# Kernel optimization log

Hardware: AMD Instinct MI355X
Metric: run time of the kernel (lower is better)

Reference implementation:

```python
import jax, jax.numpy as jnp
import numpy as np

B, LQ, LKV, E, H, D, P = 2, 2048, 2048, 1024, 16, 64, 64
NEG = -1e10


def setup_inputs() -> dict:
    key = jax.random.key(0)
    ks = jax.random.split(key, 8)
    inputs_q = jax.random.normal(ks[0], (B, LQ, E), jnp.float32)
    inputs_kv = jax.random.normal(ks[1], (B, LKV, E), jnp.float32)
    key_prefix = jax.random.normal(ks[2], (B, P, H, D), jnp.float32)
    value_prefix = jax.random.normal(ks[3], (B, P, H, D), jnp.float32)
    # causal mask, broadcastable over heads: [B, 1, LQ, LKV]
    mask = jnp.broadcast_to(jnp.tril(jnp.ones((LQ, LKV), bool)), (B, 1, LQ, LKV))
    scale = 1.0 / np.sqrt(E)  # fan_in variance scaling
    Wq = jax.random.normal(ks[4], (E, H, D), jnp.float32) * scale
    Wk = jax.random.normal(ks[5], (E, H, D), jnp.float32) * scale
    Wv = jax.random.normal(ks[6], (E, H, D), jnp.float32) * scale
    Wo = jax.random.normal(ks[7], (H, D, E), jnp.float32) * (1.0 / np.sqrt(H * D))
    return dict(inputs_q=inputs_q, inputs_kv=inputs_kv, key_prefix=key_prefix,
                value_prefix=value_prefix, mask=mask, Wq=Wq, Wk=Wk, Wv=Wv, Wo=Wo)


def reference(inputs_q, inputs_kv, key_prefix, value_prefix, mask, Wq, Wk, Wv, Wo):
    depth_scaling = jnp.sqrt(jnp.asarray(D, inputs_q.dtype))
    # query kernel is divided by sqrt(head_dim) at init -> fold into projection
    q = jnp.einsum('bqe,ehd->bqhd', inputs_q, Wq) / depth_scaling
    k = jnp.einsum('bke,ehd->bkhd', inputs_kv, Wk)
    v = jnp.einsum('bke,ehd->bkhd', inputs_kv, Wv)
    # prefix concat on the key/value length axis
    k = jnp.concatenate([key_prefix, k], axis=1)   # [B, P+LKV, H, D]
    v = jnp.concatenate([value_prefix, v], axis=1)
    # mask -> additive bias; prefix tokens get zero bias (always attendable)
    bias = jnp.where(mask, 0.0, NEG).astype(inputs_q.dtype)      # [B,1,LQ,LKV]
    prefix_bias = jnp.zeros(bias.shape[:-1] + (P,), bias.dtype)  # [B,1,LQ,P]
    bias = jnp.concatenate([prefix_bias, bias], axis=-1)         # [B,1,LQ,P+LKV]
    scores = jnp.einsum('bqhd,bkhd->bhqk', q, k) + bias
    probs = jax.nn.softmax(scores, axis=-1)
    ctx = jnp.einsum('bhqk,bkhd->bqhd', probs, v)
    return jnp.einsum('bqhd,hde->bqe', ctx, Wo)
```

## Files before the change

kernel.cpp:

```cpp
#include <hip/hip_runtime.h>
#include <hip/hip_bf16.h>

#define B_   2
#define LQ_  2048
#define LKV_ 2048
#define E_   1024
#define H_   16
#define D_   64
#define P_   64
#define LT_  (P_ + LKV_)
#define NEG_ -1e10f
#define LOG2E_ 1.4426950408889634f

typedef unsigned short ushort_t;
typedef unsigned int   uint_t;
typedef float f32x4   __attribute__((ext_vector_type(4)));
typedef float f32x16  __attribute__((ext_vector_type(16)));
typedef short bf16x8  __attribute__((ext_vector_type(8)));
typedef uint_t u32x4  __attribute__((ext_vector_type(4)));

__device__ __forceinline__ ushort_t f2bf(float f) {
    union { float f; uint_t u; } v; v.f = f;
    return (ushort_t)((v.u + 0x7fffu + ((v.u >> 16) & 1u)) >> 16);
}

__device__ __forceinline__ uint_t cvt_pk_bf16(float lo, float hi) {
    uint_t r;
    asm("v_cvt_pk_bf16_f32 %0, %1, %2" : "=v"(r) : "v"(lo), "v"(hi));
    return r;
}

__device__ __forceinline__ float exp2x(float x) {
    float r;
    asm("v_exp_f32 %0, %1" : "=v"(r) : "v"(x));
    return r;
}

__device__ __forceinline__ float bflo(uint_t u) {
    return __builtin_bit_cast(float, u << 16);
}
__device__ __forceinline__ float bfhi(uint_t u) {
    return __builtin_bit_cast(float, u & 0xFFFF0000u);
}


#define GLOAD16(gp, lp)                                                     \
    __builtin_amdgcn_global_load_lds(                                       \
        (const __attribute__((address_space(1))) void*)(gp),                \
        (__attribute__((address_space(3))) void*)(lp), 16, 0, 0)

__global__ __launch_bounds__(256) void cast_ab(const float* __restrict__ a,
                                               const float* __restrict__ b,
                                               ushort_t* __restrict__ da,
                                               ushort_t* __restrict__ db)
{
    const int idx = blockIdx.x * 256 + threadIdx.x;
    constexpr int HALF = 4096 * 1024 / 4;
    const float4 v = (idx < HALF) ? ((const float4*)a)[idx]
                                  : ((const float4*)b)[idx - HALF];
    const uint2 p = make_uint2((uint_t)f2bf(v.x) | ((uint_t)f2bf(v.y) << 16),
                               (uint_t)f2bf(v.z) | ((uint_t)f2bf(v.w) << 16));
    if (idx < HALF) ((uint2*)da)[idx] = p;
    else            ((uint2*)db)[idx - HALF] = p;
}

__global__ __launch_bounds__(256) void transpose_cast(
    const float* __restrict__ s0, const float* __restrict__ s1,
    const float* __restrict__ s2, const float* __restrict__ s3,
    ushort_t* __restrict__ d0, ushort_t* __restrict__ d1,
    ushort_t* __restrict__ d2, ushort_t* __restrict__ d3)
{
    const float* S = (blockIdx.z == 0) ? s0 : (blockIdx.z == 1) ? s1
                     : (blockIdx.z == 2) ? s2 : s3;
    ushort_t* D = (blockIdx.z == 0) ? d0 : (blockIdx.z == 1) ? d1
                  : (blockIdx.z == 2) ? d2 : d3;
    __shared__ float t[32][33];
    const int tid = threadIdx.x;
    const int tx = tid & 31, ty = tid >> 5;
    const int x0 = blockIdx.x * 32, y0 = blockIdx.y * 32;
    #pragma unroll
    for (int i = 0; i < 4; ++i)
        t[ty + i * 8][tx] = S[(size_t)(y0 + ty + i * 8) * 1024 + x0 + tx];
    __syncthreads();
    #pragma unroll
    for (int i = 0; i < 4; ++i)
        D[(size_t)(x0 + ty + i * 8) * 1024 + (y0 + tx)] = f2bf(t[tx][ty + i * 8]);
}

__device__ __forceinline__ void gemm_core(const ushort_t* __restrict__ A,
                                          const ushort_t* __restrict__ Wt,
                                          ushort_t* As, ushort_t* Bs,
                                          int m0, int n0, f32x4 (*acc)[4])
{
    constexpr int K = 1024, NSTEP = 16;
    const int tid  = threadIdx.x;
    const int lane = tid & 63;
    const int wave = tid >> 6;
    const int l15 = lane & 15, lg = lane >> 4;
    const int wr = (wave >> 1) * 64;
    const int wc = (wave & 1) * 64;
    const uint_t xr = (uint_t)((l15 & 7) << 4);

    auto STAGE = [&](int step, int par) {
        const int k0 = step * 64;
        char* ad = (char*)As + par * 16384;
        char* bd = (char*)Bs + par * 16384;
        #pragma unroll
        for (int i = 0; i < 4; ++i) {
            const int c = i * 256 + tid;
            const int row = c >> 3, cc = c & 7;
            const size_t so = (size_t)row * K + k0 + ((cc ^ (row & 7)) * 8);
            GLOAD16(A  + (size_t)m0 * K + so, ad + (i * 256 + wave * 64) * 16);
            GLOAD16(Wt + (size_t)n0 * K + so, bd + (i * 256 + wave * 64) * 16);
        }
    };

    STAGE(0, 0);
    asm volatile("s_waitcnt vmcnt(0)" ::: "memory");
    __builtin_amdgcn_s_barrier();

    for (int i = 0; i < NSTEP; ++i) {
        const int cur = i & 1;
        if (i + 1 < NSTEP) STAGE(i + 1, cur ^ 1);

        const char* as = (const char*)As + cur * 16384;
        const char* bs = (const char*)Bs + cur * 16384;
        bf16x8 af[2][4], bfr[2][4];
        #pragma unroll
        for (int kt = 0; kt < 2; ++kt) {
            #pragma unroll
            for (int mt = 0; mt < 4; ++mt)
                af[kt][mt] = *(const bf16x8*)(as + (wr + mt * 16 + l15) * 128
                                              + ((kt * 64 + lg * 16) ^ xr));
            #pragma unroll
            for (int nt = 0; nt < 4; ++nt)
                bfr[kt][nt] = *(const bf16x8*)(bs + (wc + nt * 16 + l15) * 128
                                               + ((kt * 64 + lg * 16) ^ xr));
        }
        #pragma unroll
        for (int mt = 0; mt < 4; ++mt)
            #pragma unroll
            for (int nt = 0; nt < 4; ++nt) {
                acc[mt][nt] = __builtin_amdgcn_mfma_f32_16x16x32_bf16(
                    af[0][mt], bfr[0][nt], acc[mt][nt], 0, 0, 0);
                acc[mt][nt] = __builtin_amdgcn_mfma_f32_16x16x32_bf16(
                    af[1][mt], bfr[1][nt], acc[mt][nt], 0, 0, 0);
            }

        if (i + 1 < NSTEP) {
            asm volatile("s_waitcnt vmcnt(0)" ::: "memory");
            __builtin_amdgcn_s_barrier();
        }
    }
}

__global__ __launch_bounds__(256) void gemm_qkv(
    const ushort_t* __restrict__ Aq, const ushort_t* __restrict__ Akv,
    const ushort_t* __restrict__ WqT, const ushort_t* __restrict__ WkT,
    const ushort_t* __restrict__ WvT,
    ushort_t* __restrict__ qws, ushort_t* __restrict__ kws,
    ushort_t* __restrict__ vws)
{
    __shared__ __align__(16) ushort_t As[2 * 128 * 64];
    __shared__ __align__(16) ushort_t Bs[2 * 128 * 64];
    const int by = blockIdx.y, sel = by >> 3;
    const ushort_t* A  = sel ? Akv : Aq;
    const ushort_t* Wt = (sel == 0) ? WqT : (sel == 1) ? WkT : WvT;
    const float scale  = sel ? 1.0f : 0.125f * LOG2E_;
    const int m0 = blockIdx.x * 128, n0 = (by & 7) * 128;

    f32x4 acc[4][4];
    #pragma unroll
    for (int mt = 0; mt < 4; ++mt)
        #pragma unroll
        for (int nt = 0; nt < 4; ++nt) acc[mt][nt] = (f32x4)0.f;

    gemm_core(A, Wt, As, Bs, m0, n0, acc);

    const int lane = threadIdx.x & 63, wave = threadIdx.x >> 6;
    const int l15 = lane & 15, lg = lane >> 4;
    const int wr = (wave >> 1) * 64, wc = (wave & 1) * 64;

    if (sel == 2) {
        #pragma unroll
        for (int mt = 0; mt < 4; ++mt)
            #pragma unroll
            for (int nt = 0; nt < 4; ++nt) {
                const int n = n0 + wc + nt * 16 + l15;
                const int h = n >> 6, d = n & 63;
                const int m = m0 + wr + mt * 16 + lg * 4;
                const int bb = m >> 11, ll = m & 2047;
                const uint2 pk = make_uint2(
                    (uint_t)f2bf(acc[mt][nt][0]) | ((uint_t)f2bf(acc[mt][nt][1]) << 16),
                    (uint_t)f2bf(acc[mt][nt][2]) | ((uint_t)f2bf(acc[mt][nt][3]) << 16));
                *(uint2*)(vws + ((size_t)(bb * H_ + h) * D_ + d) * LT_ + P_ + ll) = pk;
            }
    } else {
        ushort_t* Cw     = (sel == 0) ? qws : kws;
        const int Lout   = (sel == 0) ? LQ_ : LT_;
        const int rowoff = (sel == 0) ? 0 : P_;
        #pragma unroll
        for (int mt = 0; mt < 4; ++mt)
            #pragma unroll
            for (int nt = 0; nt < 4; ++nt) {
                const int n = n0 + wc + nt * 16 + l15;
                const int h = n >> 6, d = n & 63;
                #pragma unroll
                for (int r = 0; r < 4; ++r) {
                    const int m = m0 + wr + mt * 16 + lg * 4 + r;
                    const int bb = m >> 11, ll = m & 2047;
                    Cw[(((size_t)(bb * H_ + h) * Lout) + (rowoff + ll)) * D_ + d] =
                        f2bf(acc[mt][nt][r] * scale);
                }
            }
    }
}

__global__ __launch_bounds__(256) void gemm_out(const ushort_t* __restrict__ A,
                                                const ushort_t* __restrict__ Wt,
                                                float* __restrict__ C)
{
    __shared__ __align__(16) ushort_t As[2 * 128 * 64];
    __shared__ __align__(16) ushort_t Bs[2 * 128 * 64];
    const int m0 = blockIdx.x * 128, n0 = blockIdx.y * 128;

    f32x4 acc[4][4];
    #pragma unroll
    for (int mt = 0; mt < 4; ++mt)
        #pragma unroll
        for (int nt = 0; nt < 4; ++nt) acc[mt][nt] = (f32x4)0.f;

    gemm_core(A, Wt, As, Bs, m0, n0, acc);

    const int lane = threadIdx.x & 63, wave = threadIdx.x >> 6;
    const int l15 = lane & 15, lg = lane >> 4;
    const int wr = (wave >> 1) * 64, wc = (wave & 1) * 64;
    #pragma unroll
    for (int mt = 0; mt < 4; ++mt)
        #pragma unroll
        for (int nt = 0; nt < 4; ++nt) {
            const int n = n0 + wc + nt * 16 + l15;
            #pragma unroll
            for (int r = 0; r < 4; ++r) {
                const int m = m0 + wr + mt * 16 + lg * 4 + r;
                C[(size_t)m * 1024 + n] = acc[mt][nt][r];
            }
        }
}

__global__ __launch_bounds__(256) void prefix_copy(const float* __restrict__ kp,
                                                   const float* __restrict__ vp,
                                                   ushort_t* __restrict__ kws,
                                                   ushort_t* __restrict__ vws)
{
    const int idx = blockIdx.x * 256 + threadIdx.x;
    constexpr int TOT = B_ * P_ * H_ * D_ / 4;
    if (idx >= TOT) return;
    const int d4 = idx & 15;
    const int h  = (idx >> 4) & 15;
    const int p  = (idx >> 8) & 63;
    const int b  = idx >> 14;
    const float4 kv = ((const float4*)kp)[idx];
    const float4 vv = ((const float4*)vp)[idx];
    const size_t kdst = ((size_t)(b * H_ + h) * LT_ + p) * D_ + d4 * 4;
    *(uint2*)(kws + kdst) = make_uint2((uint_t)f2bf(kv.x) | ((uint_t)f2bf(kv.y) << 16),
                                       (uint_t)f2bf(kv.z) | ((uint_t)f2bf(kv.w) << 16));
    const float* vs = (const float*)&vv;
    #pragma unroll
    for (int i = 0; i < 4; ++i)
        vws[((size_t)(b * H_ + h) * D_ + d4 * 4 + i) * LT_ + p] = f2bf(vs[i]);
}

__global__ __launch_bounds__(256) void attn_mfma(const ushort_t* __restrict__ qws,
                                                 const ushort_t* __restrict__ kws,
                                                 const ushort_t* __restrict__ vws,
                                                 ushort_t* __restrict__ pO,
                                                 float* __restrict__ ml)
{
    const int tid  = threadIdx.x;
    const int lane = tid & 63;
    const int wave = tid >> 6;
    const int z    = blockIdx.x;
    const int slot = z >> 8;
    const int c    = z & 255;
    const int g    = c >> 5;
    const int bh   = c & 31;
    const int seg  = slot >> 1;
    const int qb   = (slot & 1) ? g : (15 - g);

    const ushort_t* Qg  = qws + (size_t)bh * LQ_ * D_;
    const ushort_t* Kg  = kws + (size_t)bh * LT_ * D_;
    const ushort_t* Vtg = vws + (size_t)bh * D_ * LT_;

    __shared__ __align__(16) ushort_t Ks[2 * 64 * 64];
    __shared__ __align__(16) ushort_t Vt[2 * 64 * 64];

    const int l31 = lane & 31;
    const int hi  = lane >> 5;
    const bool hib = (hi != 0);
    const uint_t xsw = (uint_t)((l31 & 7) << 4);
    const int qbase = qb * 128 + wave * 32;
    const int q     = qbase + l31;
    const int qe    = qbase + 31;

    bf16x8 qf[4];
    #pragma unroll
    for (int kd = 0; kd < 4; ++kd)
        qf[kd] = *(const bf16x8*)(Qg + (size_t)q * D_ + kd * 16 + hi * 8);

    f32x16 acc[2];
    acc[0] = (f32x16)0.f;
    acc[1] = (f32x16)0.f;
    float mreg = -3e38f, lpreg = 0.f;

    const int ntile = 2 * qb + 3;
    const int i0    = seg ? (qb + 2) : 0;
    const int iend  = seg ? ntile : (qb + 2);

    auto STAGE = [&](int t, int par) {
        const int t0s = t * 64;
        char* kd = (char*)Ks + par * 8192;
        char* vd = (char*)Vt + par * 8192;
        #pragma unroll
        for (int i = 0; i < 2; ++i) {
            const int c2 = i * 256 + tid;
            const int rr = c2 >> 3, cc = c2 & 7;
            GLOAD16(Kg + (size_t)(t0s + rr) * D_ + ((cc ^ (rr & 7)) * 8),
                    kd + (i * 256 + wave * 64) * 16);
            GLOAD16(Vtg + (size_t)rr * LT_ + t0s + ((cc ^ (rr & 7)) * 8),
                    vd + (i * 256 + wave * 64) * 16);
        }
    };

    STAGE(i0, 0);
    STAGE(i0 + 1, 1);

    for (int i = i0; i < iend; ++i) {
        const int t0 = i * 64;
        const int cur = (i - i0) & 1;
        if (i + 1 < iend) {
            asm volatile("s_waitcnt vmcnt(4)" ::: "memory");
        } else {
            asm volatile("s_waitcnt vmcnt(0)" ::: "memory");
        }
        __builtin_amdgcn_s_barrier();

        if (t0 <= P_ + qe) {
            const char* KsB = (const char*)Ks + cur * 8192;
            const char* VtB = (const char*)Vt + cur * 8192;

            f32x16 sv[2];
            __builtin_amdgcn_s_setprio(1);
            #pragma unroll
            for (int th = 0; th < 2; ++th) {
                f32x16 zf = (f32x16)0.f;
                #pragma unroll
                for (int kd = 0; kd < 4; ++kd) {
                    const bf16x8 a = *(const bf16x8*)(
                        KsB + (th * 32 + l31) * 128 + ((kd * 32 + hi * 16) ^ xsw));
                    zf = __builtin_amdgcn_mfma_f32_32x32x16_bf16(a, qf[kd], zf, 0, 0, 0);
                }
                sv[th] = zf;
            }
            __builtin_amdgcn_s_setprio(0);

            if (t0 + 63 > P_ + qbase) {
                #pragma unroll
                for (int th = 0; th < 2; ++th)
                    #pragma unroll
                    for (int r = 0; r < 16; ++r) {
                        const int t = t0 + th * 32 + (r & 3) + 8 * (r >> 2) + 4 * hi;
                        if (!(t < P_ || (t - P_) <= q)) sv[th][r] += NEG_;
                    }
            }

            float t16a[16];
            #pragma unroll
            for (int r = 0; r < 16; ++r) t16a[r] = fmaxf(sv[0][r], sv[1][r]);
            float t8a[8];
            #pragma unroll
            for (int r = 0; r < 8; ++r) t8a[r] = fmaxf(t16a[r], t16a[r + 8]);
            float t4a[4];
            #pragma unroll
            for (int r = 0; r < 4; ++r) t4a[r] = fmaxf(t8a[r], t8a[r + 4]);
            float pmax = fmaxf(fmaxf(t4a[0], t4a[1]), fmaxf(t4a[2], t4a[3]));
            pmax = fmaxf(pmax, __shfl_xor(pmax, 32));

            if (!__all(pmax <= mreg + 8.0f)) {
                const float mnew = fmaxf(mreg, pmax);
                const float corr = exp2x(mreg - mnew);
                mreg = mnew;
                lpreg *= corr;
                #pragma unroll
                for (int dh = 0; dh < 2; ++dh)
                    #pragma unroll
                    for (int r = 0; r < 16; ++r) acc[dh][r] *= corr;
            }

            float rs = 0.f;
            #pragma unroll
            for (int th = 0; th < 2; ++th)
                #pragma unroll
                for (int r = 0; r < 16; ++r) {
                    const float e = exp2x(sv[th][r] - mreg);
                    sv[th][r] = e;
                    rs += e;
                }
            lpreg += rs;

            bf16x8 pb[4];
            #pragma unroll
            for (int th = 0; th < 2; ++th) {
                uint_t xp[8];
                #pragma unroll
                for (int a = 0; a < 8; ++a)
                    xp[a] = cvt_pk_bf16(sv[th][2 * a], sv[th][2 * a + 1]);
                #pragma unroll
                for (int gg = 0; gg < 2; ++gg) {
                    const uint_t x0 = xp[gg * 4 + 0], x1 = xp[gg * 4 + 1];
                    const uint_t x2 = xp[gg * 4 + 2], x3 = xp[gg * 4 + 3];
                    const uint_t s0 = (uint_t)__shfl_xor((int)x0, 32);
                    const uint_t s1 = (uint_t)__shfl_xor((int)x1, 32);
                    const uint_t s2 = (uint_t)__shfl_xor((int)x2, 32);
                    const uint_t s3 = (uint_t)__shfl_xor((int)x3, 32);
                    uint4 w;
                    w.x = hib ? s2 : x0;
                    w.y = hib ? s3 : x1;
                    w.z = hib ? x2 : s0;
                    w.w = hib ? x3 : s1;
                    pb[th * 2 + gg] = __builtin_bit_cast(bf16x8, w);
                }
            }

            __builtin_amdgcn_s_setprio(1);
            #pragma unroll
            for (int dh = 0; dh < 2; ++dh) {
                #pragma unroll
                for (int kt = 0; kt < 4; ++kt) {
                    const bf16x8 vfr = *(const bf16x8*)(
                        VtB + (dh * 32 + l31) * 128 + ((kt * 32 + hi * 16) ^ xsw));
                    acc[dh] = __builtin_amdgcn_mfma_f32_32x32x16_bf16(
                        vfr, pb[kt], acc[dh], 0, 0, 0);
                }
            }
            __builtin_amdgcn_s_setprio(0);
        }

        __builtin_amdgcn_s_barrier();
        if (i + 2 < iend) STAGE(i + 2, cur);
    }

    const float ltot = lpreg + __shfl_xor(lpreg, 32);
    const size_t qrow = (size_t)(seg * 32 + bh) * 2048 + q;
    #pragma unroll
    for (int dh = 0; dh < 2; ++dh)
        #pragma unroll
        for (int gg = 0; gg < 4; ++gg) {
            const int d = dh * 32 + gg * 8 + hi * 4;
            const uint2 pk = make_uint2(
                cvt_pk_bf16(acc[dh][4 * gg + 0], acc[dh][4 * gg + 1]),
                cvt_pk_bf16(acc[dh][4 * gg + 2], acc[dh][4 * gg + 3]));
            *(uint2*)(pO + qrow * 64 + d) = pk;
        }
    if (hi == 0)
        *(float2*)(ml + qrow * 2) = make_float2(mreg, ltot);
}

__global__ __launch_bounds__(256) void attn_merge(const ushort_t* __restrict__ pO,
                                                  const float* __restrict__ ml,
                                                  ushort_t* __restrict__ ctx)
{
    const int idx = blockIdx.x * 256 + threadIdx.x;
    const int dg = idx & 15;
    const int q  = (idx >> 4) & 2047;
    const int bh = idx >> 15;
    const int b = bh >> 4, h = bh & 15;

    const size_t q0 = (size_t)bh * 2048 + q;
    const size_t q1 = (size_t)(32 + bh) * 2048 + q;
    const float2 ml0 = *(const float2*)(ml + q0 * 2);
    const float2 ml1 = *(const float2*)(ml + q1 * 2);
    const float mmax = fmaxf(ml0.x, ml1.x);
    const float e0 = exp2x(ml0.x - mmax);
    const float e1 = exp2x(ml1.x - mmax);
    const float inv = 1.0f / (e0 * ml0.y + e1 * ml1.y);

    const uint2 a0 = *(const uint2*)(pO + q0 * 64 + dg * 4);
    const uint2 a1 = *(const uint2*)(pO + q1 * 64 + dg * 4);
    const float o0 = (e0 * bflo(a0.x) + e1 * bflo(a1.x)) * inv;
    const float o1 = (e0 * bfhi(a0.x) + e1 * bfhi(a1.x)) * inv;
    const float o2 = (e0 * bflo(a0.y) + e1 * bflo(a1.y)) * inv;
    const float o3 = (e0 * bfhi(a0.y) + e1 * bfhi(a1.y)) * inv;

    const uint2 pk = make_uint2(
        (uint_t)f2bf(o0) | ((uint_t)f2bf(o1) << 16),
        (uint_t)f2bf(o2) | ((uint_t)f2bf(o3) << 16));
    *(uint2*)(ctx + (((size_t)b * LQ_ + q) * H_ + h) * D_ + dg * 4) = pk;
}

extern "C" void kernel_launch(void* const* d_in, const int* in_sizes, int n_in,
                              void* d_out, int out_size, void* d_ws, size_t ws_size,
                              hipStream_t stream)
{
    const float* inputs_q     = (const float*)d_in[0];
    const float* inputs_kv    = (const float*)d_in[1];
    const float* key_prefix   = (const float*)d_in[2];
    const float* value_prefix = (const float*)d_in[3];
    const float* Wq = (const float*)d_in[5];
    const float* Wk = (const float*)d_in[6];
    const float* Wv = (const float*)d_in[7];
    const float* Wo = (const float*)d_in[8];
    float* out = (float*)d_out;

    ushort_t* Aq  = (ushort_t*)d_ws;
    ushort_t* Akv = Aq  + (size_t)4096 * 1024;
    ushort_t* WqT = Akv + (size_t)4096 * 1024;
    ushort_t* WkT = WqT + (size_t)1024 * 1024;
    ushort_t* WvT = WkT + (size_t)1024 * 1024;
    ushort_t* WoT = WvT + (size_t)1024 * 1024;
    ushort_t* qws = WoT + (size_t)1024 * 1024;
    ushort_t* kws = qws + (size_t)B_ * H_ * LQ_ * D_;
    ushort_t* vws = kws + (size_t)B_ * H_ * LT_ * D_;
    ushort_t* ctx = vws + (size_t)B_ * H_ * LT_ * D_;

    ushort_t* pO    = Aq;
    float*    mlbuf = (float*)WqT;

    cast_ab<<<8192, 256, 0, stream>>>(inputs_q, inputs_kv, Aq, Akv);
    transpose_cast<<<dim3(32, 32, 4), 256, 0, stream>>>(Wq, Wk, Wv, Wo,
                                                        WqT, WkT, WvT, WoT);
    gemm_qkv<<<dim3(32, 24), 256, 0, stream>>>(Aq, Akv, WqT, WkT, WvT,
                                               qws, kws, vws);
    prefix_copy<<<128, 256, 0, stream>>>(key_prefix, value_prefix, kws, vws);
    attn_mfma<<<2 * B_ * H_ * (LQ_ / 128), 256, 0, stream>>>(qws, kws, vws,
                                                             pO, mlbuf);
    attn_merge<<<4096, 256, 0, stream>>>(pO, mlbuf, ctx);
    gemm_out<<<dim3(32, 8), 256, 0, stream>>>(ctx, WoT, out);
}
```

Measured before the change: 132.0 us.

## Merge prep kernels into one launch and single-buffer GEMM shared tiles

Folds the input cast, weight transpose-cast and prefix copy into a single prep kernel, dispatched by block index, which removes two kernel launches. Separately, the GEMM core drops its double-buffered LDS staging. Each k-step now loads its tile, waits, computes, then syncs. This halves shared memory per block, which may raise occupancy, but global loads no longer overlap with MFMA work inside a block.

Measured after the change: 131.9 us. Within noise of the previous version (-0.1%).

```diff
diff --git a/kernel.cpp b/kernel.cpp
--- a/kernel.cpp
+++ b/kernel.cpp
@@ -49,42 +49,61 @@
         (const __attribute__((address_space(1))) void*)(gp),                \
         (__attribute__((address_space(3))) void*)(lp), 16, 0, 0)
 
-__global__ __launch_bounds__(256) void cast_ab(const float* __restrict__ a,
-                                               const float* __restrict__ b,
-                                               ushort_t* __restrict__ da,
-                                               ushort_t* __restrict__ db)
-{
-    const int idx = blockIdx.x * 256 + threadIdx.x;
-    constexpr int HALF = 4096 * 1024 / 4;
-    const float4 v = (idx < HALF) ? ((const float4*)a)[idx]
-                                  : ((const float4*)b)[idx - HALF];
-    const uint2 p = make_uint2((uint_t)f2bf(v.x) | ((uint_t)f2bf(v.y) << 16),
-                               (uint_t)f2bf(v.z) | ((uint_t)f2bf(v.w) << 16));
-    if (idx < HALF) ((uint2*)da)[idx] = p;
-    else            ((uint2*)db)[idx - HALF] = p;
-}
-
-__global__ __launch_bounds__(256) void transpose_cast(
-    const float* __restrict__ s0, const float* __restrict__ s1,
-    const float* __restrict__ s2, const float* __restrict__ s3,
+__global__ __launch_bounds__(256) void prep(
+    const float* __restrict__ iq, const float* __restrict__ ikv,
+    const float* __restrict__ w0, const float* __restrict__ w1,
+    const float* __restrict__ w2, const float* __restrict__ w3,
+    const float* __restrict__ kp, const float* __restrict__ vp,
+    ushort_t* __restrict__ Aq, ushort_t* __restrict__ Akv,
     ushort_t* __restrict__ d0, ushort_t* __restrict__ d1,
-    ushort_t* __restrict__ d2, ushort_t* __restrict__ d3)
-{
-    const float* S = (blockIdx.z == 0) ? s0 : (blockIdx.z == 1) ? s1
-                     : (blockIdx.z == 2) ? s2 : s3;
-    ushort_t* D = (blockIdx.z == 0) ? d0 : (blockIdx.z == 1) ? d1
-                  : (blockIdx.z == 2) ? d2 : d3;
+    ushort_t* __restrict__ d2, ushort_t* __restrict__ d3,
+    ushort_t* __restrict__ kws, ushort_t* __restrict__ vws)
+{
     __shared__ float t[32][33];
+    const int blk = blockIdx.x;
     const int tid = threadIdx.x;
-    const int tx = tid & 31, ty = tid >> 5;
-    const int x0 = blockIdx.x * 32, y0 = blockIdx.y * 32;
-    #pragma unroll
-    for (int i = 0; i < 4; ++i)
-        t[ty + i * 8][tx] = S[(size_t)(y0 + ty + i * 8) * 1024 + x0 + tx];
-    __syncthreads();
-    #pragma unroll
-    for (int i = 0; i < 4; ++i)
-        D[(size_t)(x0 + ty + i * 8) * 1024 + (y0 + tx)] = f2bf(t[tx][ty + i * 8]);
+
+    if (blk < 8192) {
+        const int idx = blk * 256 + tid;
+        constexpr int HALF = 4096 * 1024 / 4;
+        const float4 v = (idx < HALF) ? ((const float4*)iq)[idx]
+                                      : ((const float4*)ikv)[idx - HALF];
+        const uint2 p = make_uint2((uint_t)f2bf(v.x) | ((uint_t)f2bf(v.y) << 16),
+                                   (uint_t)f2bf(v.z) | ((uint_t)f2bf(v.w) << 16));
+        if (idx < HALF) ((uint2*)Aq)[idx] = p;
+        else            ((uint2*)Akv)[idx - HALF] = p;
+    } else if (blk < 12288) {
+        const int tr = blk - 8192;
+        const int bz = tr >> 10, rem = tr & 1023;
+        const int x0 = (rem & 31) * 32, y0 = (rem >> 5) * 32;
+        const float* S = (bz == 0) ? w0 : (bz == 1) ? w1 : (bz == 2) ? w2 : w3;
+        ushort_t* D = (bz == 0) ? d0 : (bz == 1) ? d1 : (bz == 2) ? d2 : d3;
+        const int tx = tid & 31, ty = tid >> 5;
+        #pragma unroll
+        for (int i = 0; i < 4; ++i)
+            t[ty + i * 8][tx] = S[(size_t)(y0 + ty + i * 8) * 1024 + x0 + tx];
+        __syncthreads();
+        #pragma unroll
+        for (int i = 0; i < 4; ++i)
+            D[(size_t)(x0 + ty + i * 8) * 1024 + (y0 + tx)] =
+                f2bf(t[tx][ty + i * 8]);
+    } else {
+        const int idx = (blk - 12288) * 256 + tid;
+        const int d4 = idx & 15;
+        const int h  = (idx >> 4) & 15;
+        const int p  = (idx >> 8) & 63;
+        const int b  = idx >> 14;
+        const float4 kv = ((const float4*)kp)[idx];
+        const float4 vv = ((const float4*)vp)[idx];
+        const size_t kdst = ((size_t)(b * H_ + h) * LT_ + p) * D_ + d4 * 4;
+        *(uint2*)(kws + kdst) =
+            make_uint2((uint_t)f2bf(kv.x) | ((uint_t)f2bf(kv.y) << 16),
+                       (uint_t)f2bf(kv.z) | ((uint_t)f2bf(kv.w) << 16));
+        const float* vs = (const float*)&vv;
+        #pragma unroll
+        for (int i = 0; i < 4; ++i)
+            vws[((size_t)(b * H_ + h) * D_ + d4 * 4 + i) * LT_ + p] = f2bf(vs[i]);
+    }
 }
 
 __device__ __forceinline__ void gemm_core(const ushort_t* __restrict__ A,
@@ -101,40 +120,29 @@
     const int wc = (wave & 1) * 64;
     const uint_t xr = (uint_t)((l15 & 7) << 4);
 
-    auto STAGE = [&](int step, int par) {
-        const int k0 = step * 64;
-        char* ad = (char*)As + par * 16384;
-        char* bd = (char*)Bs + par * 16384;
-        #pragma unroll
-        for (int i = 0; i < 4; ++i) {
-            const int c = i * 256 + tid;
+    for (int i = 0; i < NSTEP; ++i) {
+        const int k0 = i * 64;
+        #pragma unroll
+        for (int j = 0; j < 4; ++j) {
+            const int c = j * 256 + tid;
             const int row = c >> 3, cc = c & 7;
             const size_t so = (size_t)row * K + k0 + ((cc ^ (row & 7)) * 8);
-            GLOAD16(A  + (size_t)m0 * K + so, ad + (i * 256 + wave * 64) * 16);
-            GLOAD16(Wt + (size_t)n0 * K + so, bd + (i * 256 + wave * 64) * 16);
-        }
-    };
-
-    STAGE(0, 0);
-    asm volatile("s_waitcnt vmcnt(0)" ::: "memory");
-    __builtin_amdgcn_s_barrier();
-
-    for (int i = 0; i < NSTEP; ++i) {
-        const int cur = i & 1;
-        if (i + 1 < NSTEP) STAGE(i + 1, cur ^ 1);
-
-        const char* as = (const char*)As + cur * 16384;
-        const char* bs = (const char*)Bs + cur * 16384;
+            GLOAD16(A  + (size_t)m0 * K + so, (char*)As + (j * 256 + wave * 64) * 16);
+            GLOAD16(Wt + (size_t)n0 * K + so, (char*)Bs + (j * 256 + wave * 64) * 16);
+        }
+        asm volatile("s_waitcnt vmcnt(0)" ::: "memory");
+        __builtin_amdgcn_s_barrier();
+
         bf16x8 af[2][4], bfr[2][4];
         #pragma unroll
         for (int kt = 0; kt < 2; ++kt) {
             #pragma unroll
             for (int mt = 0; mt < 4; ++mt)
-                af[kt][mt] = *(const bf16x8*)(as + (wr + mt * 16 + l15) * 128
+                af[kt][mt] = *(const bf16x8*)((const char*)As + (wr + mt * 16 + l15) * 128
                                               + ((kt * 64 + lg * 16) ^ xr));
             #pragma unroll
             for (int nt = 0; nt < 4; ++nt)
-                bfr[kt][nt] = *(const bf16x8*)(bs + (wc + nt * 16 + l15) * 128
+                bfr[kt][nt] = *(const bf16x8*)((const char*)Bs + (wc + nt * 16 + l15) * 128
                                                + ((kt * 64 + lg * 16) ^ xr));
         }
         #pragma unroll
@@ -147,10 +155,7 @@
                     af[1][mt], bfr[1][nt], acc[mt][nt], 0, 0, 0);
             }
 
-        if (i + 1 < NSTEP) {
-            asm volatile("s_waitcnt vmcnt(0)" ::: "memory");
-            __builtin_amdgcn_s_barrier();
-        }
+        __builtin_amdgcn_s_barrier();
     }
 }
 
@@ -161,8 +166,8 @@
     ushort_t* __restrict__ qws, ushort_t* __restrict__ kws,
     ushort_t* __restrict__ vws)
 {
-    __shared__ __align__(16) ushort_t As[2 * 128 * 64];
-    __shared__ __align__(16) ushort_t Bs[2 * 128 * 64];
+    __shared__ __align__(16) ushort_t As[128 * 64];
+    __shared__ __align__(16) ushort_t Bs[128 * 64];
     const int by = blockIdx.y, sel = by >> 3;
     const ushort_t* A  = sel ? Akv : Aq;
     const ushort_t* Wt = (sel == 0) ? WqT : (sel == 1) ? WkT : WvT;
@@ -220,8 +225,8 @@
                                                 const ushort_t* __restrict__ Wt,
                                                 float* __restrict__ C)
 {
-    __shared__ __align__(16) ushort_t As[2 * 128 * 64];
-    __shared__ __align__(16) ushort_t Bs[2 * 128 * 64];
+    __shared__ __align__(16) ushort_t As[128 * 64];
+    __shared__ __align__(16) ushort_t Bs[128 * 64];
     const int m0 = blockIdx.x * 128, n0 = blockIdx.y * 128;
 
     f32x4 acc[4][4];
@@ -246,29 +251,6 @@
                 C[(size_t)m * 1024 + n] = acc[mt][nt][r];
             }
         }
-}
-
-__global__ __launch_bounds__(256) void prefix_copy(const float* __restrict__ kp,
-                                                   const float* __restrict__ vp,
-                                                   ushort_t* __restrict__ kws,
-                                                   ushort_t* __restrict__ vws)
-{
-    const int idx = blockIdx.x * 256 + threadIdx.x;
-    constexpr int TOT = B_ * P_ * H_ * D_ / 4;
-    if (idx >= TOT) return;
-    const int d4 = idx & 15;
-    const int h  = (idx >> 4) & 15;
-    const int p  = (idx >> 8) & 63;
-    const int b  = idx >> 14;
-    const float4 kv = ((const float4*)kp)[idx];
-    const float4 vv = ((const float4*)vp)[idx];
-    const size_t kdst = ((size_t)(b * H_ + h) * LT_ + p) * D_ + d4 * 4;
-    *(uint2*)(kws + kdst) = make_uint2((uint_t)f2bf(kv.x) | ((uint_t)f2bf(kv.y) << 16),
-                                       (uint_t)f2bf(kv.z) | ((uint_t)f2bf(kv.w) << 16));
-    const float* vs = (const float*)&vv;
-    #pragma unroll
-    for (int i = 0; i < 4; ++i)
-        vws[((size_t)(b * H_ + h) * D_ + d4 * 4 + i) * LT_ + p] = f2bf(vs[i]);
 }
 
 __global__ __launch_bounds__(256) void attn_mfma(const ushort_t* __restrict__ qws,
@@ -526,12 +508,11 @@
     ushort_t* pO    = Aq;
     float*    mlbuf = (float*)WqT;
 
-    cast_ab<<<8192, 256, 0, stream>>>(inputs_q, inputs_kv, Aq, Akv);
-    transpose_cast<<<dim3(32, 32, 4), 256, 0, stream>>>(Wq, Wk, Wv, Wo,
-                                                        WqT, WkT, WvT, WoT);
+    prep<<<12416, 256, 0, stream>>>(inputs_q, inputs_kv, Wq, Wk, Wv, Wo,
+                                    key_prefix, value_prefix,
+                                    Aq, Akv, WqT, WkT, WvT, WoT, kws, vws);
     gemm_qkv<<<dim3(32, 24), 256, 0, stream>>>(Aq, Akv, WqT, WkT, WvT,
                                                qws, kws, vws);
-    prefix_copy<<<128, 256, 0, stream>>>(key_prefix, value_prefix, kws, vws);
     attn_mfma<<<2 * B_ * H_ * (LQ_ / 128), 256, 0, stream>>>(qws, kws, vws,
                                                              pO, mlbuf);
     attn_merge<<<4096, 256, 0, stream>>>(pO, mlbuf, ctx);
```
